# Optimization experiments

Measured on AMD Instinct MI355X. Metric: run time of the kernel, lower is better.

## Reference

```python
import jax, jax.numpy as jnp
import numpy as np

COUNT, L1, L2, L3 = 8, 3072, 15, 32


def setup_inputs() -> dict:
    key = jax.random.key(0)
    ks = jax.random.split(key, 10)
    B = 16384
    x = jax.random.uniform(ks[0], (B, L1), dtype=jnp.float32)
    ls_indices = jax.random.randint(ks[1], (B,), 0, COUNT, dtype=jnp.int32)
    s = 1.0 / np.sqrt(L1)
    l1_w = jax.random.uniform(ks[2], (COUNT * (L2 + 1), L1), minval=-s, maxval=s, dtype=jnp.float32)
    l1_b = jax.random.uniform(ks[3], (COUNT * (L2 + 1),), minval=-s, maxval=s, dtype=jnp.float32)
    # l1_fact initialized to zero in the module; use small random values for a
    # meaningful numeric test (same math either way)
    l1f_w = 0.01 * jax.random.normal(ks[4], (L2 + 1, L1), dtype=jnp.float32)
    l1f_b = 0.01 * jax.random.normal(ks[5], (L2 + 1,), dtype=jnp.float32)
    s2 = 1.0 / np.sqrt(2 * L2)
    l2_w = jax.random.uniform(ks[6], (COUNT * L3, 2 * L2), minval=-s2, maxval=s2, dtype=jnp.float32)
    l2_b = jax.random.uniform(ks[7], (COUNT * L3,), minval=-s2, maxval=s2, dtype=jnp.float32)
    s3 = 1.0 / np.sqrt(L3)
    out_w = jax.random.uniform(ks[8], (COUNT, L3), minval=-s3, maxval=s3, dtype=jnp.float32)
    out_b = jnp.zeros((COUNT,), dtype=jnp.float32)
    return {"x": x, "ls_indices": ls_indices, "l1_w": l1_w, "l1_b": l1_b,
            "l1f_w": l1f_w, "l1f_b": l1f_b, "l2_w": l2_w, "l2_b": l2_b,
            "out_w": out_w, "out_b": out_b}


def _gather_bucket(dense, idx):
    # dense: [B, count, F]; idx: [B] -> [B, F]
    return jnp.take_along_axis(dense, idx[:, None, None], axis=1)[:, 0, :]


def reference(x, ls_indices, l1_w, l1_b, l1f_w, l1f_b, l2_w, l2_b, out_w, out_b):
    B = x.shape[0]
    idx = ls_indices.reshape(-1)
    # L1 stage: dense over all buckets, then gather selected bucket
    l1s = (x @ l1_w.T + l1_b).reshape(B, COUNT, L2 + 1)
    l1c = _gather_bucket(l1s, idx)                      # [B, L2+1]
    l1f = x @ l1f_w.T + l1f_b                           # [B, L2+1]
    l1c_main, l1c_out = l1c[:, :L2], l1c[:, L2:]
    l1f_main, l1f_out = l1f[:, :L2], l1f[:, L2:]
    l1x = l1c_main + l1f_main
    # squared-clipped-ReLU pair: [x^2 * 127/128, x] clamped to [0,1]
    l1x = jnp.clip(jnp.concatenate([jnp.square(l1x) * (127.0 / 128.0), l1x], axis=1), 0.0, 1.0)
    # L2 stage
    l2s = (l1x @ l2_w.T + l2_b).reshape(B, COUNT, L3)
    l2x = jnp.clip(_gather_bucket(l2s, idx), 0.0, 1.0)  # [B, L3]
    # output stage
    l3s = (l2x @ out_w.T + out_b).reshape(B, COUNT, 1)
    l3c = _gather_bucket(l3s, idx)                      # [B, 1]
    return l3c + l1f_out + l1c_out
```

## Files before the change

kernel.cpp:

```cpp
#include <hip/hip_runtime.h>
#include <stdint.h>

#define L1D 3072
#define NB 16384
#define CH 16
#define CAP 2560
#define CPB (CAP / CH)
#define NFUSED (8 * CPB)

typedef float  float4v __attribute__((ext_vector_type(4)));
typedef short  short8  __attribute__((ext_vector_type(8)));

__device__ __forceinline__ unsigned short f2bf(float f) {
  uint32_t u = __builtin_bit_cast(uint32_t, f);
  u += 0x7fffu + ((u >> 16) & 1u);
  return (unsigned short)(u >> 16);
}

__global__ void prep_kernel(const float* __restrict__ l1w, const float* __restrict__ l1b,
                            const float* __restrict__ l1fw, const float* __restrict__ l1fb,
                            const int* __restrict__ lsi,
                            unsigned short* __restrict__ cw, float* __restrict__ cb,
                            int* __restrict__ cnt, int* __restrict__ perm) {
  if (blockIdx.x < 1536) {
    const int flat = blockIdx.x * 256 + threadIdx.x;
    const int n = flat / L1D;
    const int k = flat - n * L1D;
    cw[flat] = f2bf(l1w[flat] + l1fw[(n & 15) * L1D + k]);
    if (blockIdx.x == 0 && threadIdx.x < 128)
      cb[threadIdx.x] = l1b[threadIdx.x] + l1fb[threadIdx.x & 15];
  } else {
    const int r = (blockIdx.x - 1536) * 256 + threadIdx.x;
    const int b = lsi[r];
    const int p = atomicAdd(&cnt[b * 32], 1);
    perm[b * CAP + p] = r;
  }
}

__global__ __launch_bounds__(256, 2) void fused_kernel(
    const float* __restrict__ x, const unsigned short* __restrict__ cw,
    const float* __restrict__ cb, const int* __restrict__ perm, const int* __restrict__ cnt,
    const float* __restrict__ gl2w, const float* __restrict__ gl2b,
    const float* __restrict__ goutw, const float* __restrict__ goutb,
    float* __restrict__ out) {
  const int b = blockIdx.x / CPB;
  const int local = blockIdx.x - b * CPB;
  const int cnt_b = cnt[b * 32];
  if (local * CH >= cnt_b) return;
  const int tid = threadIdx.x;
  const int lane = tid & 63;
  const int w = tid >> 6;
  const int col = lane & 15, quad = lane >> 4;

  __shared__ struct {
    float yg[4][CH][17];
    float l2w[32][31];
    float l2b[32], outw[32], bias[16];
    int   prow[CH];
  } sm;

  if (tid < 32) {
    sm.l2b[tid]  = gl2b[b * 32 + tid];
    sm.outw[tid] = goutw[b * 32 + tid];
    if (tid < CH)
      sm.prow[tid] = (local * CH + tid < cnt_b) ? perm[b * CAP + local * CH + tid] : -1;
    if (tid < 16) sm.bias[tid] = cb[b * 16 + tid];
  }
  for (int i = tid; i < 960; i += 256) {
    const int n = i / 30, k = i - n * 30;
    sm.l2w[n][k] = gl2w[(b * 32 + n) * 30 + k];
  }

  const int idx = local * CH + col;
  const int ri = (idx < cnt_b) ? perm[b * CAP + idx] : 0;
  const float* ap = x + (size_t)(ri < 0 ? 0 : ri) * L1D + w * 32 + quad * 8;
  const unsigned short* bp = cw + (size_t)(b * 16 + col) * L1D + w * 32 + quad * 8;

  float4v acc = {0.f, 0.f, 0.f, 0.f};
  float4v a0 = *(const float4v*)ap;
  float4v a1 = *(const float4v*)(ap + 4);
  short8  bf = *(const short8*)bp;
#pragma unroll 4
  for (int it = 0; it < 23; ++it) {
    const float* apn = ap + (it + 1) * 128;
    float4v na0 = *(const float4v*)apn;
    float4v na1 = *(const float4v*)(apn + 4);
    short8  nbf = *(const short8*)(bp + (it + 1) * 128);
    short8 af;
    af[0] = (short)f2bf(a0.x); af[1] = (short)f2bf(a0.y);
    af[2] = (short)f2bf(a0.z); af[3] = (short)f2bf(a0.w);
    af[4] = (short)f2bf(a1.x); af[5] = (short)f2bf(a1.y);
    af[6] = (short)f2bf(a1.z); af[7] = (short)f2bf(a1.w);
    acc = __builtin_amdgcn_mfma_f32_16x16x32_bf16(af, bf, acc, 0, 0, 0);
    a0 = na0; a1 = na1; bf = nbf;
  }
  {
    short8 af;
    af[0] = (short)f2bf(a0.x); af[1] = (short)f2bf(a0.y);
    af[2] = (short)f2bf(a0.z); af[3] = (short)f2bf(a0.w);
    af[4] = (short)f2bf(a1.x); af[5] = (short)f2bf(a1.y);
    af[6] = (short)f2bf(a1.z); af[7] = (short)f2bf(a1.w);
    acc = __builtin_amdgcn_mfma_f32_16x16x32_bf16(af, bf, acc, 0, 0, 0);
  }

#pragma unroll
  for (int rg = 0; rg < 4; ++rg) sm.yg[w][quad * 4 + rg][col] = acc[rg];
  __syncthreads();

  {
    const int r = tid >> 4, q = tid & 15;
    const int rr = sm.prow[r];
    float act[30];
#pragma unroll
    for (int c = 0; c < 15; ++c) {
      const float v = sm.yg[0][r][c] + sm.yg[1][r][c] + sm.yg[2][r][c] + sm.yg[3][r][c]
                      + sm.bias[c];
      act[c]      = fminf(v * v * (127.0f / 128.0f), 1.0f);
      act[15 + c] = fminf(fmaxf(v, 0.0f), 1.0f);
    }
    const float y15 = sm.yg[0][r][15] + sm.yg[1][r][15] + sm.yg[2][r][15] + sm.yg[3][r][15]
                      + sm.bias[15];
    float o = 0.0f;
#pragma unroll
    for (int nn = 0; nn < 2; ++nn) {
      const int n = q * 2 + nn;
      float s = sm.l2b[n];
#pragma unroll
      for (int k = 0; k < 30; ++k) s += act[k] * sm.l2w[n][k];
      s = fminf(fmaxf(s, 0.0f), 1.0f);
      o += s * sm.outw[n];
    }
    o += __shfl_down(o, 8, 16);
    o += __shfl_down(o, 4, 16);
    o += __shfl_down(o, 2, 16);
    o += __shfl_down(o, 1, 16);
    if (q == 0 && rr >= 0) out[rr] = o + y15 + goutb[b];
  }
}

extern "C" void kernel_launch(void* const* d_in, const int* in_sizes, int n_in,
                              void* d_out, int out_size, void* d_ws, size_t ws_size,
                              hipStream_t stream) {
  const float* x    = (const float*)d_in[0];
  const int*   lsi  = (const int*)d_in[1];
  const float* l1w  = (const float*)d_in[2];
  const float* l1b  = (const float*)d_in[3];
  const float* l1fw = (const float*)d_in[4];
  const float* l1fb = (const float*)d_in[5];
  const float* l2w  = (const float*)d_in[6];
  const float* l2b  = (const float*)d_in[7];
  const float* outw = (const float*)d_in[8];
  const float* outb = (const float*)d_in[9];
  float* out = (float*)d_out;

  char* ws = (char*)d_ws;
  unsigned short* cw = (unsigned short*)ws;
  float* cb  = (float*)(ws + 786432);
  int* cnt   = (int*)(ws + 786944);
  int* perm  = (int*)(ws + 787968);

  hipMemsetAsync(cnt, 0, 1024, stream);
  prep_kernel<<<1600, 256, 0, stream>>>(l1w, l1b, l1fw, l1fb, lsi, cw, cb, cnt, perm);
  fused_kernel<<<NFUSED, 256, 0, stream>>>(x, cw, cb, perm, cnt, l2w, l2b, outw, outb, out);
}
```

Measured before the change: 334.3 us.

## Compute all eight buckets densely per row tile instead of bucket-sorted gather

Drops the bucket counting and permutation (memset plus atomics) and has each workgroup take 16 consecutive rows, computing all 128 L1 outputs with eight MFMA accumulators. It then picks each row's bucket columns from shared memory. The combined bf16 weights are pre-swizzled into an MFMA-fragment layout so B loads are contiguous, and each wave covers a contiguous K quarter. This removes the scattered row gathers and the many idle or partial workgroups, at the cost of eight times the MFMA work and more register pressure.

```diff
diff --git a/kernel.cpp b/kernel.cpp
--- a/kernel.cpp
+++ b/kernel.cpp
@@ -3,10 +3,10 @@
 
 #define L1D 3072
 #define NB 16384
-#define CH 16
-#define CAP 2560
-#define CPB (CAP / CH)
-#define NFUSED (8 * CPB)
+#define BM 16
+#define NWG (NB / BM)
+#define KW 768
+#define KSTEPS 24
 
 typedef float  float4v __attribute__((ext_vector_type(4)));
 typedef short  short8  __attribute__((ext_vector_type(8)));
@@ -19,122 +19,124 @@
 
 __global__ void prep_kernel(const float* __restrict__ l1w, const float* __restrict__ l1b,
                             const float* __restrict__ l1fw, const float* __restrict__ l1fb,
-                            const int* __restrict__ lsi,
-                            unsigned short* __restrict__ cw, float* __restrict__ cb,
-                            int* __restrict__ cnt, int* __restrict__ perm) {
-  if (blockIdx.x < 1536) {
-    const int flat = blockIdx.x * 256 + threadIdx.x;
-    const int n = flat / L1D;
-    const int k = flat - n * L1D;
-    cw[flat] = f2bf(l1w[flat] + l1fw[(n & 15) * L1D + k]);
-    if (blockIdx.x == 0 && threadIdx.x < 128)
-      cb[threadIdx.x] = l1b[threadIdx.x] + l1fb[threadIdx.x & 15];
-  } else {
-    const int r = (blockIdx.x - 1536) * 256 + threadIdx.x;
-    const int b = lsi[r];
-    const int p = atomicAdd(&cnt[b * 32], 1);
-    perm[b * CAP + p] = r;
-  }
+                            unsigned short* __restrict__ cw2, float* __restrict__ cb) {
+  const int t = blockIdx.x * 256 + threadIdx.x;
+  const int n = t / 384;
+  const int k8 = (t - n * 384) * 8;
+  const float* src = l1w + (size_t)n * L1D + k8;
+  const float* fsrc = l1fw + (size_t)(n & 15) * L1D + k8;
+  float4v w0 = *(const float4v*)src;
+  float4v w1 = *(const float4v*)(src + 4);
+  float4v f0 = *(const float4v*)fsrc;
+  float4v f1 = *(const float4v*)(fsrc + 4);
+  short8 o;
+  o[0] = (short)f2bf(w0.x + f0.x); o[1] = (short)f2bf(w0.y + f0.y);
+  o[2] = (short)f2bf(w0.z + f0.z); o[3] = (short)f2bf(w0.w + f0.w);
+  o[4] = (short)f2bf(w1.x + f1.x); o[5] = (short)f2bf(w1.y + f1.y);
+  o[6] = (short)f2bf(w1.z + f1.z); o[7] = (short)f2bf(w1.w + f1.w);
+  const int j = n >> 4, colm = n & 15;
+  const int ksg = k8 >> 5, quad = (k8 >> 3) & 3;
+  *(short8*)&cw2[(size_t)((j * 96 + ksg) * 512 + (quad * 16 + colm) * 8)] = o;
+  if (blockIdx.x == 0 && threadIdx.x < 128)
+    cb[threadIdx.x] = l1b[threadIdx.x] + l1fb[threadIdx.x & 15];
 }
 
 __global__ __launch_bounds__(256, 2) void fused_kernel(
-    const float* __restrict__ x, const unsigned short* __restrict__ cw,
-    const float* __restrict__ cb, const int* __restrict__ perm, const int* __restrict__ cnt,
+    const float* __restrict__ x, const int* __restrict__ lsi,
+    const unsigned short* __restrict__ cw2, const float* __restrict__ cb,
     const float* __restrict__ gl2w, const float* __restrict__ gl2b,
     const float* __restrict__ goutw, const float* __restrict__ goutb,
     float* __restrict__ out) {
-  const int b = blockIdx.x / CPB;
-  const int local = blockIdx.x - b * CPB;
-  const int cnt_b = cnt[b * 32];
-  if (local * CH >= cnt_b) return;
   const int tid = threadIdx.x;
   const int lane = tid & 63;
   const int w = tid >> 6;
-  const int col = lane & 15, quad = lane >> 4;
+  const int colm = lane & 15, quad = lane >> 4;
+  const int rowbase = blockIdx.x * BM;
 
-  __shared__ struct {
-    float yg[4][CH][17];
-    float l2w[32][31];
-    float l2b[32], outw[32], bias[16];
-    int   prow[CH];
-  } sm;
+  __shared__ float yg[4][BM][130];
+  __shared__ float biassm[128];
+  __shared__ int   lsb[BM];
 
-  if (tid < 32) {
-    sm.l2b[tid]  = gl2b[b * 32 + tid];
-    sm.outw[tid] = goutw[b * 32 + tid];
-    if (tid < CH)
-      sm.prow[tid] = (local * CH + tid < cnt_b) ? perm[b * CAP + local * CH + tid] : -1;
-    if (tid < 16) sm.bias[tid] = cb[b * 16 + tid];
-  }
-  for (int i = tid; i < 960; i += 256) {
-    const int n = i / 30, k = i - n * 30;
-    sm.l2w[n][k] = gl2w[(b * 32 + n) * 30 + k];
-  }
+  if (tid < 128) biassm[tid] = cb[tid];
+  if (tid < BM)  lsb[tid] = lsi[rowbase + tid];
 
-  const int idx = local * CH + col;
-  const int ri = (idx < cnt_b) ? perm[b * CAP + idx] : 0;
-  const float* ap = x + (size_t)(ri < 0 ? 0 : ri) * L1D + w * 32 + quad * 8;
-  const unsigned short* bp = cw + (size_t)(b * 16 + col) * L1D + w * 32 + quad * 8;
+  const float* ap = x + (size_t)(rowbase + colm) * L1D + w * KW + quad * 8;
+  const unsigned short* bp = cw2 + (size_t)lane * 8;
 
-  float4v acc = {0.f, 0.f, 0.f, 0.f};
+  float4v acc[8];
+#pragma unroll
+  for (int j = 0; j < 8; ++j) acc[j] = float4v{0.f, 0.f, 0.f, 0.f};
+
   float4v a0 = *(const float4v*)ap;
   float4v a1 = *(const float4v*)(ap + 4);
-  short8  bf = *(const short8*)bp;
-#pragma unroll 4
-  for (int it = 0; it < 23; ++it) {
-    const float* apn = ap + (it + 1) * 128;
-    float4v na0 = *(const float4v*)apn;
-    float4v na1 = *(const float4v*)(apn + 4);
-    short8  nbf = *(const short8*)(bp + (it + 1) * 128);
+  short8 bcur[8];
+#pragma unroll
+  for (int j = 0; j < 8; ++j)
+    bcur[j] = *(const short8*)(bp + (size_t)(j * 96 + w * 24) * 512);
+
+  for (int it = 0; it < KSTEPS; ++it) {
+    float4v na0, na1;
+    short8 nb[8];
+    if (it + 1 < KSTEPS) {
+      const float* apn = ap + (it + 1) * 32;
+      na0 = *(const float4v*)apn;
+      na1 = *(const float4v*)(apn + 4);
+#pragma unroll
+      for (int j = 0; j < 8; ++j)
+        nb[j] = *(const short8*)(bp + (size_t)(j * 96 + w * 24 + it + 1) * 512);
+    }
     short8 af;
     af[0] = (short)f2bf(a0.x); af[1] = (short)f2bf(a0.y);
     af[2] = (short)f2bf(a0.z); af[3] = (short)f2bf(a0.w);
     af[4] = (short)f2bf(a1.x); af[5] = (short)f2bf(a1.y);
     af[6] = (short)f2bf(a1.z); af[7] = (short)f2bf(a1.w);
-    acc = __builtin_amdgcn_mfma_f32_16x16x32_bf16(af, bf, acc, 0, 0, 0);
-    a0 = na0; a1 = na1; bf = nbf;
-  }
-  {
-    short8 af;
-    af[0] = (short)f2bf(a0.x); af[1] = (short)f2bf(a0.y);
-    af[2] = (short)f2bf(a0.z); af[3] = (short)f2bf(a0.w);
-    af[4] = (short)f2bf(a1.x); af[5] = (short)f2bf(a1.y);
-    af[6] = (short)f2bf(a1.z); af[7] = (short)f2bf(a1.w);
-    acc = __builtin_amdgcn_mfma_f32_16x16x32_bf16(af, bf, acc, 0, 0, 0);
+#pragma unroll
+    for (int j = 0; j < 8; ++j)
+      acc[j] = __builtin_amdgcn_mfma_f32_16x16x32_bf16(af, bcur[j], acc[j], 0, 0, 0);
+    if (it + 1 < KSTEPS) {
+      a0 = na0; a1 = na1;
+#pragma unroll
+      for (int j = 0; j < 8; ++j) bcur[j] = nb[j];
+    }
   }
 
 #pragma unroll
-  for (int rg = 0; rg < 4; ++rg) sm.yg[w][quad * 4 + rg][col] = acc[rg];
+  for (int j = 0; j < 8; ++j)
+#pragma unroll
+    for (int rg = 0; rg < 4; ++rg)
+      yg[w][quad * 4 + rg][j * 16 + colm] = acc[j][rg];
   __syncthreads();
 
   {
     const int r = tid >> 4, q = tid & 15;
-    const int rr = sm.prow[r];
+    const int b = lsb[r];
+    const int c0 = b * 16;
     float act[30];
 #pragma unroll
     for (int c = 0; c < 15; ++c) {
-      const float v = sm.yg[0][r][c] + sm.yg[1][r][c] + sm.yg[2][r][c] + sm.yg[3][r][c]
-                      + sm.bias[c];
+      const float v = yg[0][r][c0 + c] + yg[1][r][c0 + c] + yg[2][r][c0 + c]
+                      + yg[3][r][c0 + c] + biassm[c0 + c];
       act[c]      = fminf(v * v * (127.0f / 128.0f), 1.0f);
       act[15 + c] = fminf(fmaxf(v, 0.0f), 1.0f);
     }
-    const float y15 = sm.yg[0][r][15] + sm.yg[1][r][15] + sm.yg[2][r][15] + sm.yg[3][r][15]
-                      + sm.bias[15];
+    const float y15 = yg[0][r][c0 + 15] + yg[1][r][c0 + 15] + yg[2][r][c0 + 15]
+                      + yg[3][r][c0 + 15] + biassm[c0 + 15];
     float o = 0.0f;
 #pragma unroll
     for (int nn = 0; nn < 2; ++nn) {
       const int n = q * 2 + nn;
-      float s = sm.l2b[n];
+      const float* wrow = gl2w + (size_t)(b * 32 + n) * 30;
+      float s = gl2b[b * 32 + n];
 #pragma unroll
-      for (int k = 0; k < 30; ++k) s += act[k] * sm.l2w[n][k];
+      for (int k = 0; k < 30; ++k) s += act[k] * wrow[k];
       s = fminf(fmaxf(s, 0.0f), 1.0f);
-      o += s * sm.outw[n];
+      o += s * goutw[b * 32 + n];
     }
     o += __shfl_down(o, 8, 16);
     o += __shfl_down(o, 4, 16);
     o += __shfl_down(o, 2, 16);
     o += __shfl_down(o, 1, 16);
-    if (q == 0 && rr >= 0) out[rr] = o + y15 + goutb[b];
+    if (q == 0) out[rowbase + r] = o + y15 + goutb[b];
   }
 }
 
@@ -154,12 +156,9 @@
   float* out = (float*)d_out;
 
   char* ws = (char*)d_ws;
-  unsigned short* cw = (unsigned short*)ws;
-  float* cb  = (float*)(ws + 786432);
-  int* cnt   = (int*)(ws + 786944);
-  int* perm  = (int*)(ws + 787968);
+  unsigned short* cw2 = (unsigned short*)ws;
+  float* cb = (float*)(ws + 786432);
 
-  hipMemsetAsync(cnt, 0, 1024, stream);
-  prep_kernel<<<1600, 256, 0, stream>>>(l1w, l1b, l1fw, l1fb, lsi, cw, cb, cnt, perm);
-  fused_kernel<<<NFUSED, 256, 0, stream>>>(x, cw, cb, perm, cnt, l2w, l2b, outw, outb, out);
+  prep_kernel<<<192, 256, 0, stream>>>(l1w, l1b, l1fw, l1fb, cw2, cb);
+  fused_kernel<<<NWG, 256, 0, stream>>>(x, lsi, cw2, cb, l2w, l2b, outw, outb, out);
 }
```

Result: faster. 326.0 us (-2.5%).
